# Performance work log

Hardware: AMD Instinct MI355X
Metric: run time of the kernel (lower is better)

The kernel has to match this reference:

```python
import jax, jax.numpy as jnp
import numpy as np

HOP = 2  # init kwarg

def setup_inputs() -> dict:
    N, D, E = 100000, 64, 1600000
    key = jax.random.key(0)
    k1, k2, k3 = jax.random.split(key, 3)
    x = jax.random.normal(k1, (N, D), dtype=jnp.float32)
    row = jax.random.randint(k2, (E,), 0, N, dtype=jnp.int32)
    col = jax.random.randint(k3, (E,), 0, N, dtype=jnp.int32)
    # degree of each destination node, consistent with the adjacency; clamp >=1
    counts = jax.ops.segment_sum(jnp.ones((E,), dtype=jnp.float32), row, num_segments=N)
    deg = jnp.maximum(counts, 1.0).reshape(N, 1)
    return {"x": x, "deg": deg, "row": row, "col": col}

def reference(x, deg, row, col):
    N, D = x.shape
    degrev = jnp.reciprocal(deg)                      # [N,1]
    # feature augmentation: [N, 3D]
    x3 = jnp.concatenate((x, x * jax.lax.rsqrt(deg), x * jnp.sqrt(deg)), axis=1)

    def spmm(v):  # (adj_t @ v)[i] = sum_{(i,j) in edges} v[j]
        return jax.ops.segment_sum(v[col], row, num_segments=N)

    xs = [x3, degrev * spmm(x3)]
    for _ in range(2, HOP + 1):
        xs.append(degrev * spmm(xs[-1]) - xs[-2])
    # [N, 3D*(hop+1)] -> [N, 3(hop+1), D] -> [N, D, 3(hop+1)]
    out = jnp.concatenate(xs, axis=1).reshape(N, -1, D).transpose(0, 2, 1)
    return out
```

## Files before the change

kernel.cpp:

```cpp
#include <hip/hip_runtime.h>


static inline size_t ws_align(size_t x) { return (x + 255) & ~(size_t)255; }

typedef float vfloat4 __attribute__((ext_vector_type(4)));

__device__ inline float bf2f(unsigned short s) {
  return __uint_as_float(((unsigned)s) << 16);
}
__device__ inline unsigned short f2bf(float f) {
  unsigned u = __float_as_uint(f);
  unsigned r = u + 0x7fff + ((u >> 16) & 1);
  return (unsigned short)(r >> 16);
}
__device__ inline float bflo(unsigned p) { return __uint_as_float(p << 16); }
__device__ inline float bfhi(unsigned p) { return __uint_as_float(p & 0xffff0000u); }
__device__ inline unsigned packbf(float a, float b) {
  return (unsigned)f2bf(a) | ((unsigned)f2bf(b) << 16);
}
__device__ inline float sel4(float u0, float u1, float u2, float u3, int k) {
  float a = (k & 1) ? u1 : u0;
  float b = (k & 1) ? u3 : u2;
  return (k & 2) ? b : a;
}

__global__ __launch_bounds__(1024) void k_blocksum(const float* __restrict__ deg,
                                                   int* __restrict__ partial, int N) {
  __shared__ int wsum[16];
  int t = threadIdx.x;
  int idx = blockIdx.x * 1024 + t;
  int v = (idx < N) ? (int)(deg[idx] + 0.5f) : 0;
  for (int off = 32; off; off >>= 1) v += __shfl_down(v, off, 64);
  if ((t & 63) == 0) wsum[t >> 6] = v;
  __syncthreads();
  if (t == 0) {
    int s = 0;
#pragma unroll
    for (int k = 0; k < 16; ++k) s += wsum[k];
    partial[blockIdx.x] = s;
  }
}

__global__ void k_scanpartial(const int* __restrict__ partial,
                              int* __restrict__ pscan, int NB) {
  __shared__ int buf[1024];
  int t = threadIdx.x;
  for (int k = t; k < NB; k += blockDim.x) buf[k] = partial[k];
  __syncthreads();
  if (t == 0) {
    int run = 0;
    for (int k = 0; k < NB; ++k) { int v = buf[k]; buf[k] = run; run += v; }
  }
  __syncthreads();
  for (int k = t; k < NB; k += blockDim.x) pscan[k] = buf[k];
}

__global__ __launch_bounds__(1024) void k_scanapply(const float* __restrict__ deg,
    const int* __restrict__ pscan, int* __restrict__ offsets,
    int* __restrict__ cursor, int N) {
  __shared__ int wsum[16];
  int t = threadIdx.x, lane = t & 63, wv = t >> 6;
  int idx = blockIdx.x * 1024 + t;
  int v = (idx < N) ? (int)(deg[idx] + 0.5f) : 0;
  int x = v;
#pragma unroll
  for (int off = 1; off < 64; off <<= 1) {
    int y = __shfl_up(x, off, 64);
    if (lane >= off) x += y;
  }
  if (lane == 63) wsum[wv] = x;
  __syncthreads();
  if (t == 0) {
    int run = 0;
#pragma unroll
    for (int k = 0; k < 16; ++k) { int s = wsum[k]; wsum[k] = run; run += s; }
  }
  __syncthreads();
  int excl = pscan[blockIdx.x] + wsum[wv] + x - v;
  if (idx < N) { offsets[idx] = excl; cursor[idx] = excl; }
}

__global__ __launch_bounds__(256) void k_scatter_cvt(const float4* __restrict__ x4,
    uint2* __restrict__ xb2, const int* __restrict__ row,
    const int* __restrict__ col, int* __restrict__ cursor,
    int* __restrict__ csr, int E, int n4) {
  int i = blockIdx.x * 256 + threadIdx.x;
  if (i < n4) {
    float4 v = x4[i];
    uint2 p;
    p.x = packbf(v.x, v.y);
    p.y = packbf(v.z, v.w);
    xb2[i] = p;
  }
  if (i < E) {
    int r = row[i];
    int pos = atomicAdd(&cursor[r], 1);
    csr[pos] = col[i];
  }
}

__global__ __launch_bounds__(256) void k_prop1(const uint2* __restrict__ xb2,
    const float* __restrict__ deg, const int* __restrict__ offsets,
    const int* __restrict__ ends, const int* __restrict__ csr,
    uint4* __restrict__ xs1a4, uint2* __restrict__ xs1b2, int N) {
  int w = (blockIdx.x * 256 + threadIdx.x) >> 6;
  int lane = threadIdx.x & 63;
  if (w >= N) return;
  int q = lane & 15;
  int g = lane >> 4;
  int beg = offsets[w];
  int end = ends[w];
  float degw = deg[w];
  float s0[4] = {0.f, 0.f, 0.f, 0.f};
  float s1[4] = {0.f, 0.f, 0.f, 0.f};
  float s2[4] = {0.f, 0.f, 0.f, 0.f};
  int base = beg;
  for (; base + 16 <= end; base += 16) {
    int j0 = csr[base + g];
    int j1 = csr[base + 4 + g];
    int j2 = csr[base + 8 + g];
    int j3 = csr[base + 12 + g];
    uint2 v0 = xb2[(size_t)j0 * 16 + q];
    uint2 v1 = xb2[(size_t)j1 * 16 + q];
    uint2 v2 = xb2[(size_t)j2 * 16 + q];
    uint2 v3 = xb2[(size_t)j3 * 16 + q];
    float d0 = deg[j0], d1 = deg[j1], d2 = deg[j2], d3 = deg[j3];
    float r0 = rsqrtf(d0), r1 = rsqrtf(d1), r2 = rsqrtf(d2), r3 = rsqrtf(d3);
    float p0 = d0 * r0, p1 = d1 * r1, p2 = d2 * r2, p3 = d3 * r3;
    float f00 = bflo(v0.x), f01 = bfhi(v0.x), f02 = bflo(v0.y), f03 = bfhi(v0.y);
    float f10 = bflo(v1.x), f11 = bfhi(v1.x), f12 = bflo(v1.y), f13 = bfhi(v1.y);
    float f20 = bflo(v2.x), f21 = bfhi(v2.x), f22 = bflo(v2.y), f23 = bfhi(v2.y);
    float f30 = bflo(v3.x), f31 = bfhi(v3.x), f32 = bflo(v3.y), f33 = bfhi(v3.y);
    s0[0] += (f00 + f10) + (f20 + f30);
    s0[1] += (f01 + f11) + (f21 + f31);
    s0[2] += (f02 + f12) + (f22 + f32);
    s0[3] += (f03 + f13) + (f23 + f33);
    s1[0] = fmaf(f30, r3, fmaf(f20, r2, fmaf(f10, r1, fmaf(f00, r0, s1[0]))));
    s1[1] = fmaf(f31, r3, fmaf(f21, r2, fmaf(f11, r1, fmaf(f01, r0, s1[1]))));
    s1[2] = fmaf(f32, r3, fmaf(f22, r2, fmaf(f12, r1, fmaf(f02, r0, s1[2]))));
    s1[3] = fmaf(f33, r3, fmaf(f23, r2, fmaf(f13, r1, fmaf(f03, r0, s1[3]))));
    s2[0] = fmaf(f30, p3, fmaf(f20, p2, fmaf(f10, p1, fmaf(f00, p0, s2[0]))));
    s2[1] = fmaf(f31, p3, fmaf(f21, p2, fmaf(f11, p1, fmaf(f01, p0, s2[1]))));
    s2[2] = fmaf(f32, p3, fmaf(f22, p2, fmaf(f12, p1, fmaf(f02, p0, s2[2]))));
    s2[3] = fmaf(f33, p3, fmaf(f23, p2, fmaf(f13, p1, fmaf(f03, p0, s2[3]))));
  }
  if (base < end) {
    int e0 = base + g, e1 = base + 4 + g, e2 = base + 8 + g, e3 = base + 12 + g;
    bool b0 = e0 < end, b1 = e1 < end, b2 = e2 < end, b3 = e3 < end;
    int j0 = csr[b0 ? e0 : beg];
    int j1 = csr[b1 ? e1 : beg];
    int j2 = csr[b2 ? e2 : beg];
    int j3 = csr[b3 ? e3 : beg];
    uint2 v0 = xb2[(size_t)j0 * 16 + q];
    uint2 v1 = xb2[(size_t)j1 * 16 + q];
    uint2 v2 = xb2[(size_t)j2 * 16 + q];
    uint2 v3 = xb2[(size_t)j3 * 16 + q];
    float d0 = deg[j0], d1 = deg[j1], d2 = deg[j2], d3 = deg[j3];
    float m0 = b0 ? 1.f : 0.f, m1 = b1 ? 1.f : 0.f;
    float m2 = b2 ? 1.f : 0.f, m3 = b3 ? 1.f : 0.f;
    float r0 = rsqrtf(d0) * m0, r1 = rsqrtf(d1) * m1;
    float r2 = rsqrtf(d2) * m2, r3 = rsqrtf(d3) * m3;
    float p0 = d0 * r0, p1 = d1 * r1, p2 = d2 * r2, p3 = d3 * r3;
    float f00 = bflo(v0.x), f01 = bfhi(v0.x), f02 = bflo(v0.y), f03 = bfhi(v0.y);
    float f10 = bflo(v1.x), f11 = bfhi(v1.x), f12 = bflo(v1.y), f13 = bfhi(v1.y);
    float f20 = bflo(v2.x), f21 = bfhi(v2.x), f22 = bflo(v2.y), f23 = bfhi(v2.y);
    float f30 = bflo(v3.x), f31 = bfhi(v3.x), f32 = bflo(v3.y), f33 = bfhi(v3.y);
    s0[0] = fmaf(f30, m3, fmaf(f20, m2, fmaf(f10, m1, fmaf(f00, m0, s0[0]))));
    s0[1] = fmaf(f31, m3, fmaf(f21, m2, fmaf(f11, m1, fmaf(f01, m0, s0[1]))));
    s0[2] = fmaf(f32, m3, fmaf(f22, m2, fmaf(f12, m1, fmaf(f02, m0, s0[2]))));
    s0[3] = fmaf(f33, m3, fmaf(f23, m2, fmaf(f13, m1, fmaf(f03, m0, s0[3]))));
    s1[0] = fmaf(f30, r3, fmaf(f20, r2, fmaf(f10, r1, fmaf(f00, r0, s1[0]))));
    s1[1] = fmaf(f31, r3, fmaf(f21, r2, fmaf(f11, r1, fmaf(f01, r0, s1[1]))));
    s1[2] = fmaf(f32, r3, fmaf(f22, r2, fmaf(f12, r1, fmaf(f02, r0, s1[2]))));
    s1[3] = fmaf(f33, r3, fmaf(f23, r2, fmaf(f13, r1, fmaf(f03, r0, s1[3]))));
    s2[0] = fmaf(f30, p3, fmaf(f20, p2, fmaf(f10, p1, fmaf(f00, p0, s2[0]))));
    s2[1] = fmaf(f31, p3, fmaf(f21, p2, fmaf(f11, p1, fmaf(f01, p0, s2[1]))));
    s2[2] = fmaf(f32, p3, fmaf(f22, p2, fmaf(f12, p1, fmaf(f02, p0, s2[2]))));
    s2[3] = fmaf(f33, p3, fmaf(f23, p2, fmaf(f13, p1, fmaf(f03, p0, s2[3]))));
  }
#pragma unroll
  for (int k = 0; k < 4; ++k) {
    s0[k] += __shfl_xor(s0[k], 16, 64); s0[k] += __shfl_xor(s0[k], 32, 64);
    s1[k] += __shfl_xor(s1[k], 16, 64); s1[k] += __shfl_xor(s1[k], 32, 64);
    s2[k] += __shfl_xor(s2[k], 16, 64); s2[k] += __shfl_xor(s2[k], 32, 64);
  }
  if (g == 0) {
    float dr = 1.0f / degw;
    uint4 A;
    A.x = packbf(s0[0] * dr, s1[0] * dr);
    A.y = packbf(s0[1] * dr, s1[1] * dr);
    A.z = packbf(s0[2] * dr, s1[2] * dr);
    A.w = packbf(s0[3] * dr, s1[3] * dr);
    uint2 B;
    B.x = (unsigned)f2bf(s2[0] * dr) | ((unsigned)f2bf(s2[1] * dr) << 16);
    B.y = (unsigned)f2bf(s2[2] * dr) | ((unsigned)f2bf(s2[3] * dr) << 16);
    xs1a4[(size_t)w * 16 + q] = A;
    xs1b2[(size_t)w * 16 + q] = B;
  }
}

__global__ __launch_bounds__(256) void k_prop2(const float* __restrict__ x,
    const float* __restrict__ deg, const int* __restrict__ offsets,
    const int* __restrict__ ends, const int* __restrict__ csr,
    const uint4* __restrict__ xs1a4, const uint2* __restrict__ xs1b2,
    const unsigned* __restrict__ xs1a, const unsigned short* __restrict__ xs1b,
    float* __restrict__ out, int N) {
  __shared__ __align__(16) float obuf[4][576];
  int w = (blockIdx.x * 256 + threadIdx.x) >> 6;
  int lane = threadIdx.x & 63;
  if (w >= N) return;
  int q = lane & 15;
  int g = lane >> 4;
  int beg = offsets[w];
  int end = ends[w];
  size_t b = (size_t)w * 64 + lane;
  float xv = __builtin_nontemporal_load(&x[b]);
  unsigned pown = xs1a[b];
  unsigned short ownb = xs1b[b];
  float degi = deg[w];
  float a0[4] = {0.f, 0.f, 0.f, 0.f};
  float a1[4] = {0.f, 0.f, 0.f, 0.f};
  float a2[4] = {0.f, 0.f, 0.f, 0.f};
  int base = beg;
  for (; base + 16 <= end; base += 16) {
    int j0 = csr[base + g];
    int j1 = csr[base + 4 + g];
    int j2 = csr[base + 8 + g];
    int j3 = csr[base + 12 + g];
    uint4 pa0 = xs1a4[(size_t)j0 * 16 + q];
    uint4 pa1 = xs1a4[(size_t)j1 * 16 + q];
    uint4 pa2 = xs1a4[(size_t)j2 * 16 + q];
    uint4 pa3 = xs1a4[(size_t)j3 * 16 + q];
    uint2 pb0 = xs1b2[(size_t)j0 * 16 + q];
    uint2 pb1 = xs1b2[(size_t)j1 * 16 + q];
    uint2 pb2 = xs1b2[(size_t)j2 * 16 + q];
    uint2 pb3 = xs1b2[(size_t)j3 * 16 + q];
    a0[0] += (bflo(pa0.x) + bflo(pa1.x)) + (bflo(pa2.x) + bflo(pa3.x));
    a0[1] += (bflo(pa0.y) + bflo(pa1.y)) + (bflo(pa2.y) + bflo(pa3.y));
    a0[2] += (bflo(pa0.z) + bflo(pa1.z)) + (bflo(pa2.z) + bflo(pa3.z));
    a0[3] += (bflo(pa0.w) + bflo(pa1.w)) + (bflo(pa2.w) + bflo(pa3.w));
    a1[0] += (bfhi(pa0.x) + bfhi(pa1.x)) + (bfhi(pa2.x) + bfhi(pa3.x));
    a1[1] += (bfhi(pa0.y) + bfhi(pa1.y)) + (bfhi(pa2.y) + bfhi(pa3.y));
    a1[2] += (bfhi(pa0.z) + bfhi(pa1.z)) + (bfhi(pa2.z) + bfhi(pa3.z));
    a1[3] += (bfhi(pa0.w) + bfhi(pa1.w)) + (bfhi(pa2.w) + bfhi(pa3.w));
    a2[0] += (bflo(pb0.x) + bflo(pb1.x)) + (bflo(pb2.x) + bflo(pb3.x));
    a2[1] += (bfhi(pb0.x) + bfhi(pb1.x)) + (bfhi(pb2.x) + bfhi(pb3.x));
    a2[2] += (bflo(pb0.y) + bflo(pb1.y)) + (bflo(pb2.y) + bflo(pb3.y));
    a2[3] += (bfhi(pb0.y) + bfhi(pb1.y)) + (bfhi(pb2.y) + bfhi(pb3.y));
  }
  if (base < end) {
    int e0 = base + g, e1 = base + 4 + g, e2 = base + 8 + g, e3 = base + 12 + g;
    bool b0 = e0 < end, b1 = e1 < end, b2 = e2 < end, b3 = e3 < end;
    int j0 = csr[b0 ? e0 : beg];
    int j1 = csr[b1 ? e1 : beg];
    int j2 = csr[b2 ? e2 : beg];
    int j3 = csr[b3 ? e3 : beg];
    uint4 pa0 = xs1a4[(size_t)j0 * 16 + q];
    uint4 pa1 = xs1a4[(size_t)j1 * 16 + q];
    uint4 pa2 = xs1a4[(size_t)j2 * 16 + q];
    uint4 pa3 = xs1a4[(size_t)j3 * 16 + q];
    uint2 pb0 = xs1b2[(size_t)j0 * 16 + q];
    uint2 pb1 = xs1b2[(size_t)j1 * 16 + q];
    uint2 pb2 = xs1b2[(size_t)j2 * 16 + q];
    uint2 pb3 = xs1b2[(size_t)j3 * 16 + q];
    float m0 = b0 ? 1.f : 0.f, m1 = b1 ? 1.f : 0.f;
    float m2 = b2 ? 1.f : 0.f, m3 = b3 ? 1.f : 0.f;
    a0[0] = fmaf(bflo(pa3.x), m3, fmaf(bflo(pa2.x), m2,
             fmaf(bflo(pa1.x), m1, fmaf(bflo(pa0.x), m0, a0[0]))));
    a0[1] = fmaf(bflo(pa3.y), m3, fmaf(bflo(pa2.y), m2,
             fmaf(bflo(pa1.y), m1, fmaf(bflo(pa0.y), m0, a0[1]))));
    a0[2] = fmaf(bflo(pa3.z), m3, fmaf(bflo(pa2.z), m2,
             fmaf(bflo(pa1.z), m1, fmaf(bflo(pa0.z), m0, a0[2]))));
    a0[3] = fmaf(bflo(pa3.w), m3, fmaf(bflo(pa2.w), m2,
             fmaf(bflo(pa1.w), m1, fmaf(bflo(pa0.w), m0, a0[3]))));
    a1[0] = fmaf(bfhi(pa3.x), m3, fmaf(bfhi(pa2.x), m2,
             fmaf(bfhi(pa1.x), m1, fmaf(bfhi(pa0.x), m0, a1[0]))));
    a1[1] = fmaf(bfhi(pa3.y), m3, fmaf(bfhi(pa2.y), m2,
             fmaf(bfhi(pa1.y), m1, fmaf(bfhi(pa0.y), m0, a1[1]))));
    a1[2] = fmaf(bfhi(pa3.z), m3, fmaf(bfhi(pa2.z), m2,
             fmaf(bfhi(pa1.z), m1, fmaf(bfhi(pa0.z), m0, a1[2]))));
    a1[3] = fmaf(bfhi(pa3.w), m3, fmaf(bfhi(pa2.w), m2,
             fmaf(bfhi(pa1.w), m1, fmaf(bfhi(pa0.w), m0, a1[3]))));
    a2[0] = fmaf(bflo(pb3.x), m3, fmaf(bflo(pb2.x), m2,
             fmaf(bflo(pb1.x), m1, fmaf(bflo(pb0.x), m0, a2[0]))));
    a2[1] = fmaf(bfhi(pb3.x), m3, fmaf(bfhi(pb2.x), m2,
             fmaf(bfhi(pb1.x), m1, fmaf(bfhi(pb0.x), m0, a2[1]))));
    a2[2] = fmaf(bflo(pb3.y), m3, fmaf(bflo(pb2.y), m2,
             fmaf(bflo(pb1.y), m1, fmaf(bflo(pb0.y), m0, a2[2]))));
    a2[3] = fmaf(bfhi(pb3.y), m3, fmaf(bfhi(pb2.y), m2,
             fmaf(bfhi(pb1.y), m1, fmaf(bfhi(pb0.y), m0, a2[3]))));
  }
#pragma unroll
  for (int k = 0; k < 4; ++k) {
    a0[k] += __shfl_xor(a0[k], 16, 64); a0[k] += __shfl_xor(a0[k], 32, 64);
    a1[k] += __shfl_xor(a1[k], 16, 64); a1[k] += __shfl_xor(a1[k], 32, 64);
    a2[k] += __shfl_xor(a2[k], 16, 64); a2[k] += __shfl_xor(a2[k], 32, 64);
  }
  int src = lane >> 2;
  int k = lane & 3;
  float A0 = sel4(__shfl(a0[0], src, 64), __shfl(a0[1], src, 64),
                  __shfl(a0[2], src, 64), __shfl(a0[3], src, 64), k);
  float A1 = sel4(__shfl(a1[0], src, 64), __shfl(a1[1], src, 64),
                  __shfl(a1[2], src, 64), __shfl(a1[3], src, 64), k);
  float A2 = sel4(__shfl(a2[0], src, 64), __shfl(a2[1], src, 64),
                  __shfl(a2[2], src, 64), __shfl(a2[3], src, 64), k);
  float dr = 1.0f / degi;
  float ri = rsqrtf(degi);
  float qi = degi * ri;
  float h0 = bflo(pown);
  float h1 = bfhi(pown);
  float h2 = bf2f(ownb);
  float o0 = xv, o1 = xv * ri, o2 = xv * qi;

  float* ob = obuf[(threadIdx.x >> 6) & 3];
  ob[lane * 9 + 0] = o0;
  ob[lane * 9 + 1] = o1;
  ob[lane * 9 + 2] = o2;
  ob[lane * 9 + 3] = h0;
  ob[lane * 9 + 4] = h1;
  ob[lane * 9 + 5] = h2;
  ob[lane * 9 + 6] = A0 * dr - o0;
  ob[lane * 9 + 7] = A1 * dr - o1;
  ob[lane * 9 + 8] = A2 * dr - o2;
  __builtin_amdgcn_wave_barrier();
  vfloat4* op4 = (vfloat4*)(out + (size_t)w * 576);
#pragma unroll
  for (int it = 0; it < 2; ++it) {
    int idx = it * 64 + lane;
    vfloat4 v = *(const vfloat4*)&ob[idx * 4];
    __builtin_nontemporal_store(v, op4 + idx);
  }
  if (lane < 16) {
    int idx = 128 + lane;
    vfloat4 v = *(const vfloat4*)&ob[idx * 4];
    __builtin_nontemporal_store(v, op4 + idx);
  }
}

extern "C" void kernel_launch(void* const* d_in, const int* in_sizes, int n_in,
                              void* d_out, int out_size, void* d_ws, size_t ws_size,
                              hipStream_t stream) {
  const float* x   = (const float*)d_in[0];
  const float* deg = (const float*)d_in[1];
  const int*   row = (const int*)d_in[2];
  const int*   col = (const int*)d_in[3];
  float* out = (float*)d_out;

  int N = in_sizes[1];
  int E = in_sizes[2];
  int NB = (N + 1023) / 1024;

  char* ws = (char*)d_ws;
  size_t off = 0;
  int* offsets = (int*)(ws + off); off = ws_align(off + (size_t)N * 4);
  int* cursor  = (int*)(ws + off); off = ws_align(off + (size_t)N * 4);
  int* partial = (int*)(ws + off); off = ws_align(off + (size_t)NB * 4);
  int* pscan   = (int*)(ws + off); off = ws_align(off + (size_t)NB * 4);
  int* csr     = (int*)(ws + off); off = ws_align(off + ((size_t)E + N) * 4);
  unsigned short* xb = (unsigned short*)(ws + off); off = ws_align(off + (size_t)N * 64 * 2);
  unsigned* xs1a = (unsigned*)(ws + off); off = ws_align(off + (size_t)N * 64 * 4);
  unsigned short* xs1b = (unsigned short*)(ws + off); off = ws_align(off + (size_t)N * 64 * 2);

  k_blocksum<<<NB, 1024, 0, stream>>>(deg, partial, N);
  k_scanpartial<<<1, 128, 0, stream>>>(partial, pscan, NB);
  k_scanapply<<<NB, 1024, 0, stream>>>(deg, pscan, offsets, cursor, N);

  int n4 = N * 16;
  int mx = (E > n4) ? E : n4;
  k_scatter_cvt<<<(mx + 255) / 256, 256, 0, stream>>>((const float4*)x,
      (uint2*)xb, row, col, cursor, csr, E, n4);

  int hopBlocks = (N + 3) / 4;
  k_prop1<<<hopBlocks, 256, 0, stream>>>((const uint2*)xb, deg, offsets, cursor,
                                         csr, (uint4*)xs1a, (uint2*)xs1b, N);
  k_prop2<<<hopBlocks, 256, 0, stream>>>(x, deg, offsets, cursor, csr,
                                         (const uint4*)xs1a, (const uint2*)xs1b,
                                         xs1a, xs1b, out, N);
}
```

Before: 465.5 us.

## Replace three-kernel prefix scan with atomic per-wave segment allocation

Replaces the blocksum / single-block scan / apply sequence with one kernel in which each wavefront does an inclusive scan of its node degrees and reserves a contiguous CSR range via one atomicAdd on a global counter. This removes two kernel launches and the serial single-thread scan over block partials. Segments are no longer in node order, which the CSR consumers tolerate because they read explicit offsets. Tail-edge neighbour indices are also redirected to node 0, so masked-out gathers hit a shared line instead of a real neighbour's row.

```diff
diff --git a/kernel.cpp b/kernel.cpp
--- a/kernel.cpp
+++ b/kernel.cpp
@@ -24,43 +24,11 @@
   return (k & 2) ? b : a;
 }
 
-__global__ __launch_bounds__(1024) void k_blocksum(const float* __restrict__ deg,
-                                                   int* __restrict__ partial, int N) {
-  __shared__ int wsum[16];
-  int t = threadIdx.x;
-  int idx = blockIdx.x * 1024 + t;
-  int v = (idx < N) ? (int)(deg[idx] + 0.5f) : 0;
-  for (int off = 32; off; off >>= 1) v += __shfl_down(v, off, 64);
-  if ((t & 63) == 0) wsum[t >> 6] = v;
-  __syncthreads();
-  if (t == 0) {
-    int s = 0;
-#pragma unroll
-    for (int k = 0; k < 16; ++k) s += wsum[k];
-    partial[blockIdx.x] = s;
-  }
-}
-
-__global__ void k_scanpartial(const int* __restrict__ partial,
-                              int* __restrict__ pscan, int NB) {
-  __shared__ int buf[1024];
-  int t = threadIdx.x;
-  for (int k = t; k < NB; k += blockDim.x) buf[k] = partial[k];
-  __syncthreads();
-  if (t == 0) {
-    int run = 0;
-    for (int k = 0; k < NB; ++k) { int v = buf[k]; buf[k] = run; run += v; }
-  }
-  __syncthreads();
-  for (int k = t; k < NB; k += blockDim.x) pscan[k] = buf[k];
-}
-
-__global__ __launch_bounds__(1024) void k_scanapply(const float* __restrict__ deg,
-    const int* __restrict__ pscan, int* __restrict__ offsets,
-    int* __restrict__ cursor, int N) {
-  __shared__ int wsum[16];
-  int t = threadIdx.x, lane = t & 63, wv = t >> 6;
-  int idx = blockIdx.x * 1024 + t;
+__global__ __launch_bounds__(256) void k_alloc(const float* __restrict__ deg,
+    int* __restrict__ offsets, int* __restrict__ cursor,
+    int* __restrict__ counter, int N) {
+  int idx = blockIdx.x * 256 + threadIdx.x;
+  int lane = threadIdx.x & 63;
   int v = (idx < N) ? (int)(deg[idx] + 0.5f) : 0;
   int x = v;
 #pragma unroll
@@ -68,15 +36,10 @@
     int y = __shfl_up(x, off, 64);
     if (lane >= off) x += y;
   }
-  if (lane == 63) wsum[wv] = x;
-  __syncthreads();
-  if (t == 0) {
-    int run = 0;
-#pragma unroll
-    for (int k = 0; k < 16; ++k) { int s = wsum[k]; wsum[k] = run; run += s; }
-  }
-  __syncthreads();
-  int excl = pscan[blockIdx.x] + wsum[wv] + x - v;
+  int base = 0;
+  if (lane == 63) base = atomicAdd(counter, x);
+  base = __shfl(base, 63, 64);
+  int excl = base + x - v;
   if (idx < N) { offsets[idx] = excl; cursor[idx] = excl; }
 }
 
@@ -147,10 +110,10 @@
   if (base < end) {
     int e0 = base + g, e1 = base + 4 + g, e2 = base + 8 + g, e3 = base + 12 + g;
     bool b0 = e0 < end, b1 = e1 < end, b2 = e2 < end, b3 = e3 < end;
-    int j0 = csr[b0 ? e0 : beg];
-    int j1 = csr[b1 ? e1 : beg];
-    int j2 = csr[b2 ? e2 : beg];
-    int j3 = csr[b3 ? e3 : beg];
+    int j0 = csr[b0 ? e0 : beg]; j0 = b0 ? j0 : 0;
+    int j1 = csr[b1 ? e1 : beg]; j1 = b1 ? j1 : 0;
+    int j2 = csr[b2 ? e2 : beg]; j2 = b2 ? j2 : 0;
+    int j3 = csr[b3 ? e3 : beg]; j3 = b3 ? j3 : 0;
     uint2 v0 = xb2[(size_t)j0 * 16 + q];
     uint2 v1 = xb2[(size_t)j1 * 16 + q];
     uint2 v2 = xb2[(size_t)j2 * 16 + q];
@@ -251,10 +214,10 @@
   if (base < end) {
     int e0 = base + g, e1 = base + 4 + g, e2 = base + 8 + g, e3 = base + 12 + g;
     bool b0 = e0 < end, b1 = e1 < end, b2 = e2 < end, b3 = e3 < end;
-    int j0 = csr[b0 ? e0 : beg];
-    int j1 = csr[b1 ? e1 : beg];
-    int j2 = csr[b2 ? e2 : beg];
-    int j3 = csr[b3 ? e3 : beg];
+    int j0 = csr[b0 ? e0 : beg]; j0 = b0 ? j0 : 0;
+    int j1 = csr[b1 ? e1 : beg]; j1 = b1 ? j1 : 0;
+    int j2 = csr[b2 ? e2 : beg]; j2 = b2 ? j2 : 0;
+    int j3 = csr[b3 ? e3 : beg]; j3 = b3 ? j3 : 0;
     uint4 pa0 = xs1a4[(size_t)j0 * 16 + q];
     uint4 pa1 = xs1a4[(size_t)j1 * 16 + q];
     uint4 pa2 = xs1a4[(size_t)j2 * 16 + q];
@@ -348,22 +311,19 @@
 
   int N = in_sizes[1];
   int E = in_sizes[2];
-  int NB = (N + 1023) / 1024;
 
   char* ws = (char*)d_ws;
   size_t off = 0;
   int* offsets = (int*)(ws + off); off = ws_align(off + (size_t)N * 4);
   int* cursor  = (int*)(ws + off); off = ws_align(off + (size_t)N * 4);
-  int* partial = (int*)(ws + off); off = ws_align(off + (size_t)NB * 4);
-  int* pscan   = (int*)(ws + off); off = ws_align(off + (size_t)NB * 4);
+  int* counter = (int*)(ws + off); off = ws_align(off + 4);
   int* csr     = (int*)(ws + off); off = ws_align(off + ((size_t)E + N) * 4);
   unsigned short* xb = (unsigned short*)(ws + off); off = ws_align(off + (size_t)N * 64 * 2);
   unsigned* xs1a = (unsigned*)(ws + off); off = ws_align(off + (size_t)N * 64 * 4);
   unsigned short* xs1b = (unsigned short*)(ws + off); off = ws_align(off + (size_t)N * 64 * 2);
 
-  k_blocksum<<<NB, 1024, 0, stream>>>(deg, partial, N);
-  k_scanpartial<<<1, 128, 0, stream>>>(partial, pscan, NB);
-  k_scanapply<<<NB, 1024, 0, stream>>>(deg, pscan, offsets, cursor, N);
+  hipMemsetAsync(counter, 0, 4, stream);
+  k_alloc<<<(N + 255) / 256, 256, 0, stream>>>(deg, offsets, cursor, counter, N);
 
   int n4 = N * 16;
   int mx = (E > n4) ? E : n4;
```

After: 492.6 us. +5.8%, slower.
